# Kernel optimization log

Hardware: AMD Instinct MI355X
Metric: run time of the kernel (lower is better)

The kernel has to match this reference:

```python
import jax, jax.numpy as jnp
import numpy as np

B, S, D, H = 4, 2048, 1024, 16
DK = D // H


def setup_inputs() -> dict:
    key = jax.random.key(0)
    ks = jax.random.split(key, 12)
    std = 1.0 / np.sqrt(D)
    return {
        "query": jax.random.normal(ks[0], (B, S, D), jnp.float32),
        "key": jax.random.normal(ks[1], (B, S, D), jnp.float32),
        "value": jax.random.normal(ks[2], (B, S, D), jnp.float32),
        "fc_w": jax.random.normal(ks[3], (D, D), jnp.float32),
        "Wq": jax.random.normal(ks[4], (D, D), jnp.float32) * std,
        "bq": jax.random.normal(ks[5], (D,), jnp.float32) * 0.01,
        "Wk": jax.random.normal(ks[6], (D, D), jnp.float32) * std,
        "bk": jax.random.normal(ks[7], (D,), jnp.float32) * 0.01,
        "Wv": jax.random.normal(ks[8], (D, D), jnp.float32) * std,
        "bv": jax.random.normal(ks[9], (D,), jnp.float32) * 0.01,
        "Wo": jax.random.normal(ks[10], (D, D), jnp.float32) * std,
        "bo": jax.random.normal(ks[11], (D,), jnp.float32) * 0.01,
    }


def reference(query, key, value, fc_w, Wq, bq, Wk, bk, Wv, bv, Wo, bo):
    b = query.shape[0]
    # meta-modulated (scaling) query projection: x @ (fc_w * base_w) + b
    q = jnp.matmul(query, fc_w * Wq) + bq
    k = jnp.matmul(key, Wk) + bk
    v = jnp.matmul(value, Wv) + bv
    # [B, S, D] -> [B, H, S, DK]
    q = q.reshape(b, -1, H, DK).transpose(0, 2, 1, 3)
    k = k.reshape(b, -1, H, DK).transpose(0, 2, 1, 3)
    v = v.reshape(b, -1, H, DK).transpose(0, 2, 1, 3)
    scores = jnp.einsum("bhqd,bhkd->bhqk", q, k) / jnp.sqrt(jnp.float32(DK))
    attn = jax.nn.softmax(scores, axis=-1)  # dropout identity at eval
    x = jnp.einsum("bhqk,bhkd->bhqd", attn, v)
    x = x.transpose(0, 2, 1, 3).reshape(b, -1, H * DK)
    return jnp.matmul(x, Wo) + bo
```

## Files before the change

kernel.cpp:

```cpp
#include <hip/hip_runtime.h>
#include <hip/hip_bf16.h>
#include <stdint.h>

#define BB 4
#define SS 2048
#define DD 1024
#define HH 16
#define DKK 64
#define MT (BB*SS)
#define KK DD

typedef __attribute__((ext_vector_type(8))) short bf16x8;
typedef __attribute__((ext_vector_type(4))) float f32x4;
typedef __attribute__((ext_vector_type(8))) unsigned short u16x8;

__device__ __forceinline__ unsigned short f2bf(float f){
  union { float f; unsigned u; } x; x.f = f;
  unsigned r = x.u + 0x7fffu + ((x.u >> 16) & 1u);
  return (unsigned short)(r >> 16);
}

__device__ __forceinline__ short bfc(float x){
  return (short)__builtin_bit_cast(unsigned short, (__bf16)x);
}

__device__ __forceinline__ float ex2(float x){
#if __has_builtin(__builtin_amdgcn_exp2f)
  return __builtin_amdgcn_exp2f(x);
#else
  float r;
  asm("v_exp_f32 %0, %1" : "=v"(r) : "v"(x));
  return r;
#endif
}

__device__ __forceinline__ float fm3(float a, float b, float c){
  return fmaxf(fmaxf(a, b), c);
}

__device__ __forceinline__ void gll16(const void* g, void* l){
  __builtin_amdgcn_global_load_lds(
      (const __attribute__((address_space(1))) void*)g,
      (__attribute__((address_space(3))) void*)l, 16, 0, 0);
}

__global__ __launch_bounds__(256) void cvt_bf16_3(const float* __restrict__ q,
                                                  const float* __restrict__ k,
                                                  const float* __restrict__ v,
                                                  unsigned short* __restrict__ qo,
                                                  unsigned short* __restrict__ ko,
                                                  unsigned short* __restrict__ vo){
  const float* in = blockIdx.y==0 ? q : blockIdx.y==1 ? k : v;
  unsigned short* out = blockIdx.y==0 ? qo : blockIdx.y==1 ? ko : vo;
  int i = blockIdx.x * 256 + threadIdx.x;
  const f32x4* p = (const f32x4*)in;
  f32x4 a = p[2*i], b = p[2*i+1];
  u16x8 o;
  #pragma unroll
  for (int j=0;j<4;j++){ o[j] = f2bf(a[j]); o[4+j] = f2bf(b[j]); }
  ((u16x8*)out)[i] = o;
}

__global__ __launch_bounds__(256) void prep_weights(
    const float* __restrict__ fc, const float* __restrict__ Wq,
    const float* __restrict__ Wk, const float* __restrict__ Wv,
    const float* __restrict__ Wo,
    unsigned short* __restrict__ Wqt, unsigned short* __restrict__ Wkt,
    unsigned short* __restrict__ Wvt, unsigned short* __restrict__ Wot){
  __shared__ float tile[32][33];
  int which = blockIdx.y;
  const float* src = which==0?Wq: which==1?Wk: which==2?Wv:Wo;
  unsigned short* dst = which==0?Wqt: which==1?Wkt: which==2?Wvt:Wot;
  int k0 = (blockIdx.x & 31)*32, n0 = (blockIdx.x >> 5)*32;
  int tid = threadIdx.x;
  #pragma unroll
  for (int i=0;i<4;i++){
    int e = tid + i*256; int r = e>>5, c = e&31;
    float v = src[(size_t)(k0+r)*DD + n0 + c];
    if (which==0) v *= fc[(size_t)(k0+r)*DD + n0 + c];
    tile[r][c] = v;
  }
  __syncthreads();
  #pragma unroll
  for (int i=0;i<4;i++){
    int e = tid + i*256; int r = e>>5, c = e&31;
    dst[(size_t)(n0+r)*DD + k0 + c] = f2bf(tile[c][r]);
  }
}

#define GEMM_BODY(EPI, A, Bt, bias, scale, Cout, m0, n0)                          \
  {                                                                               \
  const int tid = threadIdx.x;                                                    \
  const int lane = tid & 63, wid = tid >> 6;                                      \
  const int wm = wid >> 1, wn = wid & 1;                                          \
  const int g = lane >> 4, lr = lane & 15;                                        \
  f32x4 acc[4][4];                                                                \
  _Pragma("unroll")                                                               \
  for (int i=0;i<4;i++)                                                           \
    _Pragma("unroll")                                                             \
    for (int j=0;j<4;j++) acc[i][j] = (f32x4){0.f,0.f,0.f,0.f};                   \
  const char* gaBase = (const char*)((A)  + (size_t)(m0) * KK);                   \
  const char* gbBase = (const char*)((Bt) + (size_t)(n0) * KK);                   \
  auto stage = [&](int buf, int kt){                                              \
    _Pragma("unroll")                                                             \
    for (int is=0; is<2; ++is){                                                   \
      int t = is*4096 + wid*1024 + lane*16;                                       \
      int row = t >> 6, col = t & 63;                                             \
      gll16(gaBase + (size_t)row*(KK*2) + (size_t)kt*64 + col,                    \
            (char*)&Asb[buf][0] + is*4096 + wid*1024);                            \
      gll16(gbBase + (size_t)row*(KK*2) + (size_t)kt*64 + col,                    \
            (char*)&Bsb[buf][0] + is*4096 + wid*1024);                            \
    }                                                                             \
  };                                                                              \
  stage(0, 0);                                                                    \
  __syncthreads();                                                                \
  int cur = 0;                                                                    \
  for (int kt = 0; kt < KK/32; ++kt){                                             \
    if (kt + 1 < KK/32) stage(cur^1, kt+1);                                       \
    bf16x8 af[4], bfr[4];                                                         \
    _Pragma("unroll")                                                             \
    for (int f=0; f<4; ++f){                                                      \
      int ar = wm*64 + f*16 + lr;                                                 \
      af[f]  = *(const bf16x8*)&Asb[cur][ar*32 + g*8];                            \
      int br = wn*64 + f*16 + lr;                                                 \
      bfr[f] = *(const bf16x8*)&Bsb[cur][br*32 + g*8];                            \
    }                                                                             \
    _Pragma("unroll")                                                             \
    for (int i=0;i<4;i++)                                                         \
      _Pragma("unroll")                                                           \
      for (int j=0;j<4;j++)                                                       \
        acc[i][j] = __builtin_amdgcn_mfma_f32_16x16x32_bf16(af[i], bfr[j], acc[i][j], 0, 0, 0); \
    __syncthreads();                                                              \
    cur ^= 1;                                                                     \
  }                                                                               \
  _Pragma("unroll")                                                               \
  for (int j=0;j<4;j++){                                                          \
    int n = (n0) + wn*64 + j*16 + lr;                                             \
    float bv = (bias)[n];                                                         \
    _Pragma("unroll")                                                             \
    for (int i=0;i<4;i++){                                                        \
      int mbase = (m0) + wm*64 + i*16 + g*4;                                      \
      _Pragma("unroll")                                                           \
      for (int r=0;r<4;r++){                                                      \
        int m = mbase + r;                                                        \
        float v = (acc[i][j][r] + bv) * (scale);                                  \
        if (EPI == 0){                                                            \
          int b = m >> 11, s = m & (SS-1);                                        \
          int h = n >> 6, dk = n & 63;                                            \
          ((unsigned short*)(Cout))[(((size_t)(b*HH + h))*SS + s)*DKK + dk] = f2bf(v); \
        } else {                                                                  \
          ((float*)(Cout))[(size_t)m*DD + n] = v;                                 \
        }                                                                         \
      }                                                                           \
    }                                                                             \
  }                                                                               \
  }

__global__ __launch_bounds__(256) void gemm_qkv(
    const unsigned short* __restrict__ Aq, const unsigned short* __restrict__ Ak,
    const unsigned short* __restrict__ Av,
    const unsigned short* __restrict__ Wq, const unsigned short* __restrict__ Wk,
    const unsigned short* __restrict__ Wv,
    const float* __restrict__ bq, const float* __restrict__ bk,
    const float* __restrict__ bv, float qscale,
    unsigned short* __restrict__ Qo, unsigned short* __restrict__ Ko,
    unsigned short* __restrict__ Vo){
  __shared__ __align__(16) unsigned short Asb[2][128*32];
  __shared__ __align__(16) unsigned short Bsb[2][128*32];
  const int u = blockIdx.x;
  const int which = u % 3, v = u / 3;
  const int xcd = v & 7, jj = v >> 3;
  const int by = xcd*8 + (jj>>3), bx = jj & 7;
  const int m0 = by * 128, n0 = bx * 128;
  const unsigned short* A  = which==0 ? Aq : which==1 ? Ak : Av;
  const unsigned short* Bt = which==0 ? Wq : which==1 ? Wk : Wv;
  const float* bias        = which==0 ? bq : which==1 ? bk : bv;
  unsigned short* C        = which==0 ? Qo : which==1 ? Ko : Vo;
  float scale = which==0 ? qscale : 1.0f;
  GEMM_BODY(0, A, Bt, bias, scale, C, m0, n0)
}

__global__ __launch_bounds__(256) void gemm_o(
    const unsigned short* __restrict__ A, const unsigned short* __restrict__ Bt,
    const float* __restrict__ bias, float* __restrict__ Cout){
  __shared__ __align__(16) unsigned short Asb[2][128*32];
  __shared__ __align__(16) unsigned short Bsb[2][128*32];
  const int sidx = blockIdx.x;
  const int xcd = sidx & 7, jj = sidx >> 3;
  const int by = xcd*8 + (jj>>3), bx = jj & 7;
  const int m0 = by * 128, n0 = bx * 128;
  GEMM_BODY(1, A, Bt, bias, 1.0f, Cout, m0, n0)
}

__global__ __launch_bounds__(256) void transpose_v(const unsigned short* __restrict__ V,
                                                   unsigned short* __restrict__ Vt){
  __shared__ unsigned short t[64][72];
  int bh = blockIdx.y; int s0 = blockIdx.x*64;
  const unsigned short* src = V + ((size_t)bh*SS + s0)*DKK;
  int tid = threadIdx.x;
  #pragma unroll
  for (int i=0;i<2;i++){
    int e = (tid + i*256)*8; int r = e>>6, c = e&63;
    int rp = (r & 35) | ((r & 12) << 1) | ((r & 16) >> 2);
    u16x8 v = *(const u16x8*)(src + (size_t)r*DKK + c);
    #pragma unroll
    for (int j=0;j<8;j++) t[c+j][rp] = v[j];
  }
  __syncthreads();
  unsigned short* dst = Vt + ((size_t)bh*DKK)*SS + s0;
  #pragma unroll
  for (int i=0;i<2;i++){
    int e = (tid + i*256)*8; int d = e>>6, c = e&63;
    u16x8 v = *(const u16x8*)(&t[d][c]);
    *(u16x8*)(dst + (size_t)d*SS + c) = v;
  }
}

__global__ __launch_bounds__(256) void attn(
    const unsigned short* __restrict__ Qg,
    const unsigned short* __restrict__ Kg,
    const unsigned short* __restrict__ Vtg,
    unsigned short* __restrict__ Xg){
  __shared__ __align__(16) unsigned short Ks[2][64*64];
  __shared__ __align__(16) unsigned short Vs[2][64*64];
  const int tid = threadIdx.x;
  const int lane = tid & 63, wid = tid >> 6;
  const int g = lane >> 4, lr = lane & 15;
  const int u0 = blockIdx.x;
  const int wk = (u0 & 7) * 128 + (u0 >> 3);
  const int bh = wk >> 4;
  const int q0 = (wk & 15) * 128;

  const unsigned short* Qrow = Qg + ((size_t)bh*SS + q0)*DKK;
  const char* Kbase = (const char*)(Kg + (size_t)bh*SS*DKK);
  const char* Vbase = (const char*)(Vtg + (size_t)bh*DKK*SS);

  auto stageK = [&](int buf, int it){
    const char* gk = Kbase + (size_t)it*8192;
    #pragma unroll
    for (int is=0; is<2; ++is){
      int t = is*4096 + wid*1024 + lane*16;
      int row = t >> 7;
      int col = (t & 127) ^ ((row & 7) << 4);
      gll16(gk + row*128 + col, (char*)&Ks[buf][0] + is*4096 + wid*1024);
    }
  };
  auto stageV = [&](int buf, int it){
    #pragma unroll
    for (int is=0; is<2; ++is){
      int t = is*4096 + wid*1024 + lane*16;
      int row = t >> 7;
      int col = (t & 127) ^ ((row & 7) << 4);
      gll16(Vbase + (size_t)row*(SS*2) + (size_t)it*128 + col,
            (char*)&Vs[buf][0] + is*4096 + wid*1024);
    }
  };

  bf16x8 qf[2][2];
  #pragma unroll
  for (int u=0; u<2; ++u){
    int qrow = wid*32 + u*16 + lr;
    #pragma unroll
    for (int h2=0; h2<2; ++h2)
      qf[u][h2] = *(const bf16x8*)(Qrow + (size_t)qrow*DKK + g*8 + h2*32);
  }
  stageK(0, 0); stageV(0, 0);

  f32x4 Xf[2][4];
  #pragma unroll
  for (int u=0; u<2; ++u)
    #pragma unroll
    for (int d=0; d<4; ++d) Xf[u][d] = (f32x4){0.f,0.f,0.f,0.f};
  const f32x4 Zv = (f32x4){0.f,0.f,0.f,0.f};
  float m2[2] = {-1e30f, -1e30f}, ell[2] = {0.f, 0.f};
  const int sw2 = (lr & 7) << 4;

  auto body = [&](int cbuf){
    const char* Kb = (const char*)&Ks[cbuf][0];
    const char* Vb = (const char*)&Vs[cbuf][0];
    f32x4 st[4][2];
    __builtin_amdgcn_s_setprio(1);
    #pragma unroll
    for (int s4=0; s4<4; ++s4){
      int rb = (s4*16 + lr) * 128;
      bf16x8 k0 = *(const bf16x8*)(Kb + rb + ((g*16     ) ^ sw2));
      bf16x8 k1 = *(const bf16x8*)(Kb + rb + ((g*16 + 64) ^ sw2));
      st[s4][0] = __builtin_amdgcn_mfma_f32_16x16x32_bf16(k0, qf[0][0], Zv,        0,0,0);
      st[s4][0] = __builtin_amdgcn_mfma_f32_16x16x32_bf16(k1, qf[0][1], st[s4][0], 0,0,0);
      st[s4][1] = __builtin_amdgcn_mfma_f32_16x16x32_bf16(k0, qf[1][0], Zv,        0,0,0);
      st[s4][1] = __builtin_amdgcn_mfma_f32_16x16x32_bf16(k1, qf[1][1], st[s4][1], 0,0,0);
    }
    __builtin_amdgcn_s_setprio(0);

    bf16x8 pa[2][2];
    #pragma unroll
    for (int u=0; u<2; ++u){
      float t0 = fm3(st[0][u][0], st[0][u][1], st[0][u][2]);
      float t1 = fm3(st[0][u][3], st[1][u][0], st[1][u][1]);
      float t2 = fm3(st[1][u][2], st[1][u][3], st[2][u][0]);
      float t3 = fm3(st[2][u][1], st[2][u][2], st[2][u][3]);
      float t4 = fm3(st[3][u][0], st[3][u][1], st[3][u][2]);
      float tmax = fm3(fm3(t0, t1, t2), fmaxf(t3, t4), st[3][u][3]);
      tmax = fmaxf(tmax, __shfl_xor(tmax, 16));
      tmax = fmaxf(tmax, __shfl_xor(tmax, 32));
      if (__any(tmax > m2[u] + 8.f)){
        float mn = fmaxf(m2[u], tmax);
        float sc = ex2(m2[u] - mn);
        m2[u] = mn;
        ell[u] *= sc;
        #pragma unroll
        for (int r=0; r<4; ++r){
          float scr = __shfl(sc, g*4 + r);
          #pragma unroll
          for (int d=0; d<4; ++d) Xf[u][d][r] *= scr;
        }
      }
      #pragma unroll
      for (int s4=0; s4<4; ++s4)
        #pragma unroll
        for (int r=0; r<4; ++r) st[s4][u][r] = ex2(st[s4][u][r] - m2[u]);
      float ps0 = (st[0][u][0]+st[0][u][1]) + (st[0][u][2]+st[0][u][3]);
      float ps1 = (st[1][u][0]+st[1][u][1]) + (st[1][u][2]+st[1][u][3]);
      float ps2 = (st[2][u][0]+st[2][u][1]) + (st[2][u][2]+st[2][u][3]);
      float ps3 = (st[3][u][0]+st[3][u][1]) + (st[3][u][2]+st[3][u][3]);
      ell[u] += (ps0+ps1) + (ps2+ps3);
      #pragma unroll
      for (int j=0; j<8; ++j){
        pa[u][0][j] = bfc(st[(j>>2)    ][u][j&3]);
        pa[u][1][j] = bfc(st[2 + (j>>2)][u][j&3]);
      }
    }

    __builtin_amdgcn_s_setprio(1);
    #pragma unroll
    for (int d=0; d<4; ++d){
      int rb = (d*16 + lr) * 128;
      bf16x8 b0 = *(const bf16x8*)(Vb + rb + ((g*16     ) ^ sw2));
      bf16x8 b1 = *(const bf16x8*)(Vb + rb + ((g*16 + 64) ^ sw2));
      Xf[0][d] = __builtin_amdgcn_mfma_f32_16x16x32_bf16(pa[0][0], b0, Xf[0][d], 0,0,0);
      Xf[0][d] = __builtin_amdgcn_mfma_f32_16x16x32_bf16(pa[0][1], b1, Xf[0][d], 0,0,0);
      Xf[1][d] = __builtin_amdgcn_mfma_f32_16x16x32_bf16(pa[1][0], b0, Xf[1][d], 0,0,0);
      Xf[1][d] = __builtin_amdgcn_mfma_f32_16x16x32_bf16(pa[1][1], b1, Xf[1][d], 0,0,0);
    }
    __builtin_amdgcn_s_setprio(0);
  };

  for (int it = 0; it < SS/64; it += 2){
    __builtin_amdgcn_s_barrier();
    stageK(1, it+1); stageV(1, it+1);
    asm volatile("s_waitcnt vmcnt(4)" ::: "memory");
    __builtin_amdgcn_s_barrier();
    __builtin_amdgcn_sched_barrier(0);
    body(0);
    __builtin_amdgcn_s_barrier();
    if (it + 2 < SS/64){
      stageK(0, it+2); stageV(0, it+2);
      asm volatile("s_waitcnt vmcnt(4)" ::: "memory");
    } else {
      asm volatile("s_waitcnt vmcnt(0)" ::: "memory");
    }
    __builtin_amdgcn_s_barrier();
    __builtin_amdgcn_sched_barrier(0);
    body(1);
  }

  int b = bh >> 4, h = bh & 15;
  #pragma unroll
  for (int u=0; u<2; ++u){
    float elt = ell[u];
    elt += __shfl_xor(elt, 16);
    elt += __shfl_xor(elt, 32);
    float rinv[4];
    #pragma unroll
    for (int r=0; r<4; ++r) rinv[r] = 1.0f / __shfl(elt, g*4 + r);
    #pragma unroll
    for (int d=0; d<4; ++d)
      #pragma unroll
      for (int r=0; r<4; ++r){
        int s = q0 + wid*32 + u*16 + g*4 + r;
        int col = h*64 + d*16 + lr;
        Xg[((size_t)b*SS + s)*DD + col] = f2bf(Xf[u][d][r] * rinv[r]);
      }
  }
}

extern "C" void kernel_launch(void* const* d_in, const int* in_sizes, int n_in,
                              void* d_out, int out_size, void* d_ws, size_t ws_size,
                              hipStream_t stream){
  (void)in_sizes; (void)n_in; (void)out_size; (void)ws_size;
  const float* query = (const float*)d_in[0];
  const float* key   = (const float*)d_in[1];
  const float* value = (const float*)d_in[2];
  const float* fc_w  = (const float*)d_in[3];
  const float* Wq    = (const float*)d_in[4];
  const float* bq    = (const float*)d_in[5];
  const float* Wk    = (const float*)d_in[6];
  const float* bk    = (const float*)d_in[7];
  const float* Wv    = (const float*)d_in[8];
  const float* bv    = (const float*)d_in[9];
  const float* Wo    = (const float*)d_in[10];
  const float* bo    = (const float*)d_in[11];

  char* ws = (char*)d_ws;
  const size_t EL = (size_t)BB*SS*DD;
  size_t off = 0;
  auto alloc = [&](size_t bytes){ size_t o = off; off += (bytes + 255) & ~(size_t)255; return o; };
  unsigned short* qb  = (unsigned short*)(ws + alloc(EL*2));
  unsigned short* kb  = (unsigned short*)(ws + alloc(EL*2));
  unsigned short* vb  = (unsigned short*)(ws + alloc(EL*2));
  unsigned short* Wqt = (unsigned short*)(ws + alloc((size_t)DD*DD*2));
  unsigned short* Wkt = (unsigned short*)(ws + alloc((size_t)DD*DD*2));
  unsigned short* Wvt = (unsigned short*)(ws + alloc((size_t)DD*DD*2));
  unsigned short* Wot = (unsigned short*)(ws + alloc((size_t)DD*DD*2));
  unsigned short* Qh  = (unsigned short*)(ws + alloc(EL*2));
  unsigned short* Kh  = (unsigned short*)(ws + alloc(EL*2));
  unsigned short* Vh  = (unsigned short*)(ws + alloc(EL*2));
  unsigned short* Vth = vb;
  unsigned short* Xh  = qb;

  const float SC2 = 0.18033688011112042f;

  const int nbCvt = (int)(EL / 8 / 256);
  cvt_bf16_3<<<dim3(nbCvt, 3), 256, 0, stream>>>(query, key, value, qb, kb, vb);
  prep_weights<<<dim3(1024, 4), 256, 0, stream>>>(fc_w, Wq, Wk, Wv, Wo, Wqt, Wkt, Wvt, Wot);

  gemm_qkv<<<1536, 256, 0, stream>>>(qb, kb, vb, Wqt, Wkt, Wvt, bq, bk, bv, SC2,
                                     Qh, Kh, Vh);

  transpose_v<<<dim3(SS/64, BB*HH), 256, 0, stream>>>(Vh, Vth);
  attn<<<dim3(SS/128 * BB*HH), 256, 0, stream>>>(Qh, Kh, Vth, Xh);

  gemm_o<<<512, 256, 0, stream>>>(Xh, Wot, bo, (float*)d_out);
}
```

Before: 384.8 us.

## Halve attention query tile to 64 rows, rotate KV start, restructure pipeline

```diff
diff --git a/kernel.cpp b/kernel.cpp
--- a/kernel.cpp
+++ b/kernel.cpp
@@ -13,6 +13,7 @@
 typedef __attribute__((ext_vector_type(8))) short bf16x8;
 typedef __attribute__((ext_vector_type(4))) float f32x4;
 typedef __attribute__((ext_vector_type(8))) unsigned short u16x8;
+typedef __attribute__((ext_vector_type(4))) unsigned int u32x4;
 
 __device__ __forceinline__ unsigned short f2bf(float f){
   union { float f; unsigned u; } x; x.f = f;
@@ -20,8 +21,10 @@
   return (unsigned short)(r >> 16);
 }
 
-__device__ __forceinline__ short bfc(float x){
-  return (short)__builtin_bit_cast(unsigned short, (__bf16)x);
+__device__ __forceinline__ unsigned cvtpk(float lo, float hi){
+  unsigned r;
+  asm("v_cvt_pk_bf16_f32 %0, %1, %2" : "=v"(r) : "v"(lo), "v"(hi));
+  return r;
 }
 
 __device__ __forceinline__ float ex2(float x){
@@ -168,8 +171,9 @@
   __shared__ __align__(16) unsigned short Asb[2][128*32];
   __shared__ __align__(16) unsigned short Bsb[2][128*32];
   const int u = blockIdx.x;
-  const int which = u % 3, v = u / 3;
-  const int xcd = v & 7, jj = v >> 3;
+  const int which = u >> 9;
+  const int sidx = u & 511;
+  const int xcd = sidx & 7, jj = sidx >> 3;
   const int by = xcd*8 + (jj>>3), bx = jj & 7;
   const int m0 = by * 128, n0 = bx * 128;
   const unsigned short* A  = which==0 ? Aq : which==1 ? Ak : Av;
@@ -227,161 +231,148 @@
   const int lane = tid & 63, wid = tid >> 6;
   const int g = lane >> 4, lr = lane & 15;
   const int u0 = blockIdx.x;
-  const int wk = (u0 & 7) * 128 + (u0 >> 3);
-  const int bh = wk >> 4;
-  const int q0 = (wk & 15) * 128;
+  const int wk = (u0 & 7) * 256 + (u0 >> 3);
+  const int bh = wk >> 5;
+  const int q0 = (wk & 31) * 64;
+  const int rot = wk & 31;
 
   const unsigned short* Qrow = Qg + ((size_t)bh*SS + q0)*DKK;
   const char* Kbase = (const char*)(Kg + (size_t)bh*SS*DKK);
   const char* Vbase = (const char*)(Vtg + (size_t)bh*DKK*SS);
 
+  const int t0 = wid*1024 + lane*16;
+  const int t1 = 4096 + t0;
+  const int r0 = t0 >> 7, r1 = t1 >> 7;
+  const int cA0 = (t0 & 127) ^ ((r0 & 7) << 4);
+  const int cA1 = (t1 & 127) ^ ((r1 & 7) << 4);
+  const int ksrc0 = r0*128 + cA0,      ksrc1 = r1*128 + cA1;
+  const int vsrc0 = r0*(SS*2) + cA0,   vsrc1 = r1*(SS*2) + cA1;
+
   auto stageK = [&](int buf, int it){
     const char* gk = Kbase + (size_t)it*8192;
-    #pragma unroll
-    for (int is=0; is<2; ++is){
-      int t = is*4096 + wid*1024 + lane*16;
-      int row = t >> 7;
-      int col = (t & 127) ^ ((row & 7) << 4);
-      gll16(gk + row*128 + col, (char*)&Ks[buf][0] + is*4096 + wid*1024);
-    }
+    gll16(gk + ksrc0, (char*)&Ks[buf][0] + t0);
+    gll16(gk + ksrc1, (char*)&Ks[buf][0] + t1);
   };
   auto stageV = [&](int buf, int it){
-    #pragma unroll
-    for (int is=0; is<2; ++is){
-      int t = is*4096 + wid*1024 + lane*16;
-      int row = t >> 7;
-      int col = (t & 127) ^ ((row & 7) << 4);
-      gll16(Vbase + (size_t)row*(SS*2) + (size_t)it*128 + col,
-            (char*)&Vs[buf][0] + is*4096 + wid*1024);
-    }
+    const char* gv = Vbase + (size_t)it*128;
+    gll16(gv + vsrc0, (char*)&Vs[buf][0] + t0);
+    gll16(gv + vsrc1, (char*)&Vs[buf][0] + t1);
   };
 
-  bf16x8 qf[2][2];
-  #pragma unroll
-  for (int u=0; u<2; ++u){
-    int qrow = wid*32 + u*16 + lr;
-    #pragma unroll
-    for (int h2=0; h2<2; ++h2)
-      qf[u][h2] = *(const bf16x8*)(Qrow + (size_t)qrow*DKK + g*8 + h2*32);
-  }
-  stageK(0, 0); stageV(0, 0);
-
-  f32x4 Xf[2][4];
-  #pragma unroll
-  for (int u=0; u<2; ++u)
-    #pragma unroll
-    for (int d=0; d<4; ++d) Xf[u][d] = (f32x4){0.f,0.f,0.f,0.f};
+  bf16x8 qf0, qf1;
+  {
+    int qrow = wid*16 + lr;
+    qf0 = *(const bf16x8*)(Qrow + (size_t)qrow*DKK + g*8);
+    qf1 = *(const bf16x8*)(Qrow + (size_t)qrow*DKK + g*8 + 32);
+  }
+  stageK(0, rot); stageV(0, rot);
+
+  f32x4 Xf[4];
+  #pragma unroll
+  for (int d=0; d<4; ++d) Xf[d] = (f32x4){0.f,0.f,0.f,0.f};
   const f32x4 Zv = (f32x4){0.f,0.f,0.f,0.f};
-  float m2[2] = {-1e30f, -1e30f}, ell[2] = {0.f, 0.f};
+  float m2 = -1e30f, ell = 0.f;
   const int sw2 = (lr & 7) << 4;
+  const int offC0 = lr*128 + ((g*16) ^ sw2);
+  const int offC1 = lr*128 + ((g*16 + 64) ^ sw2);
+
+  __syncthreads();
 
   auto body = [&](int cbuf){
     const char* Kb = (const char*)&Ks[cbuf][0];
     const char* Vb = (const char*)&Vs[cbuf][0];
-    f32x4 st[4][2];
+    f32x4 st[4];
     __builtin_amdgcn_s_setprio(1);
     #pragma unroll
     for (int s4=0; s4<4; ++s4){
-      int rb = (s4*16 + lr) * 128;
-      bf16x8 k0 = *(const bf16x8*)(Kb + rb + ((g*16     ) ^ sw2));
-      bf16x8 k1 = *(const bf16x8*)(Kb + rb + ((g*16 + 64) ^ sw2));
-      st[s4][0] = __builtin_amdgcn_mfma_f32_16x16x32_bf16(k0, qf[0][0], Zv,        0,0,0);
-      st[s4][0] = __builtin_amdgcn_mfma_f32_16x16x32_bf16(k1, qf[0][1], st[s4][0], 0,0,0);
-      st[s4][1] = __builtin_amdgcn_mfma_f32_16x16x32_bf16(k0, qf[1][0], Zv,        0,0,0);
-      st[s4][1] = __builtin_amdgcn_mfma_f32_16x16x32_bf16(k1, qf[1][1], st[s4][1], 0,0,0);
+      bf16x8 k0 = *(const bf16x8*)(Kb + s4*2048 + offC0);
+      bf16x8 k1 = *(const bf16x8*)(Kb + s4*2048 + offC1);
+      st[s4] = __builtin_amdgcn_mfma_f32_16x16x32_bf16(k0, qf0, Zv,     0,0,0);
+      st[s4] = __builtin_amdgcn_mfma_f32_16x16x32_bf16(k1, qf1, st[s4], 0,0,0);
     }
     __builtin_amdgcn_s_setprio(0);
 
-    bf16x8 pa[2][2];
-    #pragma unroll
-    for (int u=0; u<2; ++u){
-      float t0 = fm3(st[0][u][0], st[0][u][1], st[0][u][2]);
-      float t1 = fm3(st[0][u][3], st[1][u][0], st[1][u][1]);
-      float t2 = fm3(st[1][u][2], st[1][u][3], st[2][u][0]);
-      float t3 = fm3(st[2][u][1], st[2][u][2], st[2][u][3]);
-      float t4 = fm3(st[3][u][0], st[3][u][1], st[3][u][2]);
-      float tmax = fm3(fm3(t0, t1, t2), fmaxf(t3, t4), st[3][u][3]);
-      tmax = fmaxf(tmax, __shfl_xor(tmax, 16));
-      tmax = fmaxf(tmax, __shfl_xor(tmax, 32));
-      if (__any(tmax > m2[u] + 8.f)){
-        float mn = fmaxf(m2[u], tmax);
-        float sc = ex2(m2[u] - mn);
-        m2[u] = mn;
-        ell[u] *= sc;
+    bf16x8 vb0[4], vb1[4];
+    #pragma unroll
+    for (int d=0; d<4; ++d){
+      vb0[d] = *(const bf16x8*)(Vb + d*2048 + offC0);
+      vb1[d] = *(const bf16x8*)(Vb + d*2048 + offC1);
+    }
+
+    float t0f = fm3(st[0][0], st[0][1], st[0][2]);
+    float t1f = fm3(st[0][3], st[1][0], st[1][1]);
+    float t2f = fm3(st[1][2], st[1][3], st[2][0]);
+    float t3f = fm3(st[2][1], st[2][2], st[2][3]);
+    float t4f = fm3(st[3][0], st[3][1], st[3][2]);
+    float tmax = fm3(fm3(t0f, t1f, t2f), fmaxf(t3f, t4f), st[3][3]);
+    tmax = fmaxf(tmax, __shfl_xor(tmax, 16));
+    tmax = fmaxf(tmax, __shfl_xor(tmax, 32));
+    if (__any(tmax > m2 + 8.f)){
+      float mn = fmaxf(m2, tmax);
+      float sc = ex2(m2 - mn);
+      m2 = mn;
+      ell *= sc;
+      #pragma unroll
+      for (int r=0; r<4; ++r){
+        float scr = __shfl(sc, g*4 + r);
         #pragma unroll
-        for (int r=0; r<4; ++r){
-          float scr = __shfl(sc, g*4 + r);
-          #pragma unroll
-          for (int d=0; d<4; ++d) Xf[u][d][r] *= scr;
-        }
+        for (int d=0; d<4; ++d) Xf[d][r] *= scr;
       }
+    }
+    #pragma unroll
+    for (int s4=0; s4<4; ++s4)
       #pragma unroll
-      for (int s4=0; s4<4; ++s4)
-        #pragma unroll
-        for (int r=0; r<4; ++r) st[s4][u][r] = ex2(st[s4][u][r] - m2[u]);
-      float ps0 = (st[0][u][0]+st[0][u][1]) + (st[0][u][2]+st[0][u][3]);
-      float ps1 = (st[1][u][0]+st[1][u][1]) + (st[1][u][2]+st[1][u][3]);
-      float ps2 = (st[2][u][0]+st[2][u][1]) + (st[2][u][2]+st[2][u][3]);
-      float ps3 = (st[3][u][0]+st[3][u][1]) + (st[3][u][2]+st[3][u][3]);
-      ell[u] += (ps0+ps1) + (ps2+ps3);
-      #pragma unroll
-      for (int j=0; j<8; ++j){
-        pa[u][0][j] = bfc(st[(j>>2)    ][u][j&3]);
-        pa[u][1][j] = bfc(st[2 + (j>>2)][u][j&3]);
-      }
-    }
+      for (int r=0; r<4; ++r) st[s4][r] = ex2(st[s4][r] - m2);
+    float ps0 = (st[0][0]+st[0][1]) + (st[0][2]+st[0][3]);
+    float ps1 = (st[1][0]+st[1][1]) + (st[1][2]+st[1][3]);
+    float ps2 = (st[2][0]+st[2][1]) + (st[2][2]+st[2][3]);
+    float ps3 = (st[3][0]+st[3][1]) + (st[3][2]+st[3][3]);
+    ell += (ps0+ps1) + (ps2+ps3);
+
+    u32x4 w0, w1;
+    w0[0] = cvtpk(st[0][0], st[0][1]); w0[1] = cvtpk(st[0][2], st[0][3]);
+    w0[2] = cvtpk(st[1][0], st[1][1]); w0[3] = cvtpk(st[1][2], st[1][3]);
+    w1[0] = cvtpk(st[2][0], st[2][1]); w1[1] = cvtpk(st[2][2], st[2][3]);
+    w1[2] = cvtpk(st[3][0], st[3][1]); w1[3] = cvtpk(st[3][2], st[3][3]);
+    bf16x8 pa0 = __builtin_bit_cast(bf16x8, w0);
+    bf16x8 pa1 = __builtin_bit_cast(bf16x8, w1);
 
     __builtin_amdgcn_s_setprio(1);
     #pragma unroll
     for (int d=0; d<4; ++d){
-      int rb = (d*16 + lr) * 128;
-      bf16x8 b0 = *(const bf16x8*)(Vb + rb + ((g*16     ) ^ sw2));
-      bf16x8 b1 = *(const bf16x8*)(Vb + rb + ((g*16 + 64) ^ sw2));
-      Xf[0][d] = __builtin_amdgcn_mfma_f32_16x16x32_bf16(pa[0][0], b0, Xf[0][d], 0,0,0);
-      Xf[0][d] = __builtin_amdgcn_mfma_f32_16x16x32_bf16(pa[0][1], b1, Xf[0][d], 0,0,0);
-      Xf[1][d] = __builtin_amdgcn_mfma_f32_16x16x32_bf16(pa[1][0], b0, Xf[1][d], 0,0,0);
-      Xf[1][d] = __builtin_amdgcn_mfma_f32_16x16x32_bf16(pa[1][1], b1, Xf[1][d], 0,0,0);
+      Xf[d] = __builtin_amdgcn_mfma_f32_16x16x32_bf16(pa0, vb0[d], Xf[d], 0,0,0);
+      Xf[d] = __builtin_amdgcn_mfma_f32_16x16x32_bf16(pa1, vb1[d], Xf[d], 0,0,0);
     }
     __builtin_amdgcn_s_setprio(0);
   };
 
   for (int it = 0; it < SS/64; it += 2){
-    __builtin_amdgcn_s_barrier();
-    stageK(1, it+1); stageV(1, it+1);
-    asm volatile("s_waitcnt vmcnt(4)" ::: "memory");
-    __builtin_amdgcn_s_barrier();
-    __builtin_amdgcn_sched_barrier(0);
+    { int tt = (it + 1 + rot) & 31; stageK(1, tt); stageV(1, tt); }
     body(0);
-    __builtin_amdgcn_s_barrier();
+    __syncthreads();
     if (it + 2 < SS/64){
-      stageK(0, it+2); stageV(0, it+2);
-      asm volatile("s_waitcnt vmcnt(4)" ::: "memory");
-    } else {
-      asm volatile("s_waitcnt vmcnt(0)" ::: "memory");
-    }
-    __builtin_amdgcn_s_barrier();
-    __builtin_amdgcn_sched_barrier(0);
+      int tt = (it + 2 + rot) & 31;
+      stageK(0, tt); stageV(0, tt);
+    }
     body(1);
-  }
-
+    __syncthreads();
+  }
+
+  float elt = ell;
+  elt += __shfl_xor(elt, 16);
+  elt += __shfl_xor(elt, 32);
+  float rinv[4];
+  #pragma unroll
+  for (int r=0; r<4; ++r) rinv[r] = 1.0f / __shfl(elt, g*4 + r);
   int b = bh >> 4, h = bh & 15;
   #pragma unroll
-  for (int u=0; u<2; ++u){
-    float elt = ell[u];
-    elt += __shfl_xor(elt, 16);
-    elt += __shfl_xor(elt, 32);
-    float rinv[4];
-    #pragma unroll
-    for (int r=0; r<4; ++r) rinv[r] = 1.0f / __shfl(elt, g*4 + r);
-    #pragma unroll
-    for (int d=0; d<4; ++d)
-      #pragma unroll
-      for (int r=0; r<4; ++r){
-        int s = q0 + wid*32 + u*16 + g*4 + r;
-        int col = h*64 + d*16 + lr;
-        Xg[((size_t)b*SS + s)*DD + col] = f2bf(Xf[u][d][r] * rinv[r]);
-      }
-  }
+  for (int d=0; d<4; ++d)
+    #pragma unroll
+    for (int r=0; r<4; ++r){
+      int s = q0 + wid*16 + g*4 + r;
+      int col = h*64 + d*16 + lr;
+      Xg[((size_t)b*SS + s)*DD + col] = f2bf(Xf[d][r] * rinv[r]);
+    }
 }
 
 extern "C" void kernel_launch(void* const* d_in, const int* in_sizes, int n_in,
@@ -428,7 +419,7 @@
                                      Qh, Kh, Vh);
 
   transpose_v<<<dim3(SS/64, BB*HH), 256, 0, stream>>>(Vh, Vth);
-  attn<<<dim3(SS/128 * BB*HH), 256, 0, stream>>>(Qh, Kh, Vth, Xh);
+  attn<<<2048, 256, 0, stream>>>(Qh, Kh, Vth, Xh);
 
   gemm_o<<<512, 256, 0, stream>>>(Xh, Wot, bo, (float*)d_out);
 }
```

New measurement: 380.1 us. Within noise of the previous version (-1.2%).
